# Kernel tuning notes

Measured on AMD Instinct MI355X. Metric: run time of the kernel, lower is better.

## Reference

```python
import jax, jax.numpy as jnp
import numpy as np

B, N, C, H = 16, 577, 384, 6
ONE_DIM = 24
RPD = 2 * ONE_DIM - 1  # 47
NUM_CLS = 1
HEAD_DIM = C // H
SCALE = HEAD_DIM ** -0.5


def _build_rel_pos_index():
    # Faithful to the torch loop: tmp[dy - y + off, dx - x + off] with
    # torch's negative-index wraparound -> modulo RPD.
    off = ONE_DIM // 2
    qy = np.repeat(np.arange(ONE_DIM), ONE_DIM)  # (Np,) y of each query patch
    qx = np.tile(np.arange(ONE_DIM), ONE_DIM)    # (Np,) x of each query patch
    ky, kx = qy, qx                              # key patches use same grid
    ry = (ky[None, :] - qy[:, None] + off) % RPD
    rx = (kx[None, :] - qx[:, None] + off) % RPD
    return jnp.asarray(ry * RPD + rx, dtype=jnp.int32)  # (Np, Np)


def setup_inputs() -> dict:
    key = jax.random.key(0)
    k = jax.random.split(key, 6)
    x = jax.random.normal(k[0], (B, N, C), dtype=jnp.float32)
    qkv_w = jax.random.normal(k[1], (3 * C, C), dtype=jnp.float32) * 0.02
    qkv_b = jnp.zeros((3 * C,), dtype=jnp.float32)
    proj_w = jax.random.normal(k[2], (C, C), dtype=jnp.float32) * 0.02
    proj_b = jnp.zeros((C,), dtype=jnp.float32)
    rel_pos = jax.random.normal(k[3], (H, RPD * RPD), dtype=jnp.float32) * 0.02
    mask = jax.random.randint(k[4], (B, N, N), 0, 2, dtype=jnp.int32)
    return {
        "x": x, "qkv_w": qkv_w, "qkv_b": qkv_b,
        "proj_w": proj_w, "proj_b": proj_b, "rel_pos": rel_pos,
        "rel_pos_index": _build_rel_pos_index(),
        "mask": mask, "patch_attn": 1,
    }


def reference(x, qkv_w, qkv_b, proj_w, proj_b, rel_pos, rel_pos_index, mask, patch_attn):
    # qkv projection: torch Linear -> x @ W^T + b
    qkv = x @ qkv_w.T + qkv_b                               # (B, N, 3C)
    qkv = qkv.reshape(B, N, 3, H, HEAD_DIM).transpose(2, 0, 3, 1, 4)
    q, k, v = qkv[0], qkv[1], qkv[2]                        # (B, H, N, hd)

    attn = jnp.einsum("bhqd,bhkd->bhqk", q, k) * SCALE      # (B, H, N, N)

    if patch_attn:
        # gather per-head relative-position bias for patch tokens
        bias = rel_pos[:, rel_pos_index]                    # (H, Np, Np)
        attn = attn.at[:, :, NUM_CLS:, NUM_CLS:].add(bias)

    neg = jnp.finfo(attn.dtype).min
    attn = jnp.where(mask[:, None, :, :] == 0, neg, attn)   # broadcast over heads

    attn = jax.nn.softmax(attn, axis=-1)
    out = jnp.einsum("bhqk,bhkd->bhqd", attn, v)            # (B, H, N, hd)
    out = out.transpose(0, 2, 1, 3).reshape(B, N, C)
    out = out @ proj_w.T + proj_b
    return out
```

## Files before the change

kernel.cpp:

```cpp
#include <hip/hip_runtime.h>
#include <float.h>
#include <math.h>

#define NB 16
#define NN 577
#define NC 384
#define NH 6
#define ND 64
#define RPD2 2209
#define MTOT 9232
#define MPAD 9344
#define SCALE_ 0.125f
#define NEGBIG -3.0e38f
#define BSTRIDE 580
#define NKPAD 640

typedef __attribute__((ext_vector_type(8))) short bf16x8;
typedef __attribute__((ext_vector_type(4))) float f32x4;
typedef unsigned short u16;

#define MFMA16(a, b, c) __builtin_amdgcn_mfma_f32_16x16x32_bf16(a, b, c, 0, 0, 0)

#define SQA 3932160ull
#define OFF_QH 0ull
#define OFF_QL SQA
#define OFF_KH (2ull * SQA)
#define OFF_KL (3ull * SQA)
#define OFF_VTH (4ull * SQA)
#define OFF_VTL (5ull * SQA)
#define OFF_XH (6ull * SQA)
#define OFF_XL (6ull * SQA + 3588096ull)
#define OFF_WQH (6ull * SQA + 2ull * 3588096ull)
#define OFF_WQL (OFF_WQH + 442368ull)
#define OFF_WPH (OFF_WQL + 442368ull)
#define OFF_WPL (OFF_WPH + 147456ull)
#define OFF_BT  (OFF_WPL + 147456ull)
#define OFF_PM  (OFF_BT + 2007960ull)

static __device__ __forceinline__ u16 f2bf(float f) {
  unsigned u = __float_as_uint(f);
  u += 0x7fff + ((u >> 16) & 1);
  return (u16)(u >> 16);
}
static __device__ __forceinline__ float bf2f(u16 h) {
  return __uint_as_float((unsigned)h << 16);
}
static __device__ __forceinline__ void split2(float v, u16& hi, u16& lo) {
  hi = f2bf(v);
  lo = f2bf(v - bf2f(hi));
}
static __device__ __forceinline__ void gload16(const void* g, void* l) {
  __builtin_amdgcn_global_load_lds(
      (const __attribute__((address_space(1))) void*)g,
      (__attribute__((address_space(3))) void*)l, 16, 0, 0);
}

__global__ __launch_bounds__(256) void split_inputs_k(
    const float* __restrict__ x, const float* __restrict__ wq,
    const float* __restrict__ wp, u16* __restrict__ ws)
{
  const int q = blockIdx.x * 256 + threadIdx.x;
  float4 v = {0.f, 0.f, 0.f, 0.f};
  u16 *dh, *dl;
  if (q < 897024) {
    if (q < 886272) v = ((const float4*)x)[q];
    dh = ws + OFF_XH + 4ull * q;
    dl = ws + OFF_XL + 4ull * q;
  } else if (q < 1007616) {
    int t = q - 897024;
    v = ((const float4*)wq)[t];
    dh = ws + OFF_WQH + 4ull * t;
    dl = ws + OFF_WQL + 4ull * t;
  } else {
    int t = q - 1007616;
    v = ((const float4*)wp)[t];
    dh = ws + OFF_WPH + 4ull * t;
    dl = ws + OFF_WPL + 4ull * t;
  }
  ushort4 hh, ll;
  split2(v.x, hh.x, ll.x);
  split2(v.y, hh.y, ll.y);
  split2(v.z, hh.z, ll.z);
  split2(v.w, hh.w, ll.w);
  *(ushort4*)dh = hh;
  *(ushort4*)dl = ll;
}

__global__ __launch_bounds__(256) void pack_mask_k(const int* __restrict__ mask,
                                                   unsigned* __restrict__ pm)
{
  const int wid = (blockIdx.x * 256 + threadIdx.x) >> 6;
  const int lane = threadIdx.x & 63;
  if (wid >= MTOT) return;
  const int* mr = mask + (size_t)wid * NN;
#pragma unroll
  for (int c = 0; c < 10; ++c) {
    int k = c * 64 + lane;
    int v = (k < NN) ? mr[k] : 0;
    unsigned long long bal = __ballot(v != 0);
    if (lane == 0) pm[wid * 20 + 2 * c] = (unsigned)bal;
    if (lane == 1) pm[wid * 20 + 2 * c + 1] = (unsigned)(bal >> 32);
  }
}

__global__ __launch_bounds__(256) void bias_build_k(
    const float* __restrict__ rel_pos, const int* __restrict__ rel_idx,
    const int* __restrict__ patch, u16* __restrict__ tbl)
{
  const int q = blockIdx.x;
  const int h = blockIdx.y;
  const int pa = *patch;
  u16* row = tbl + ((size_t)h * NN + q) * BSTRIDE;
  for (int kk = threadIdx.x; kk < BSTRIDE; kk += 256) {
    float v = 0.f;
    if (pa && q >= 1 && kk >= 1 && kk < NN)
      v = rel_pos[h * RPD2 + rel_idx[(q - 1) * 576 + (kk - 1)]];
    row[kk] = f2bf(v);
  }
}

__global__ __launch_bounds__(256, 3) void qkv_mfma_k(
    const u16* __restrict__ Xh, const u16* __restrict__ Xl,
    const u16* __restrict__ Wh, const u16* __restrict__ Wl,
    const float* __restrict__ bias, u16* __restrict__ ws)
{
  __shared__ u16 Ash[2][4096], Asl[2][4096];

  const int tid = threadIdx.x;
  const int w = tid >> 6, l = tid & 63, lq = l & 15, lg = l >> 4;
  const int wm = (w >> 1) * 64, wn = (w & 1) * 64;
  const int mb = blockIdx.x * 128;
  const int rb = blockIdx.y * 128;
  const int r0 = rb + wn;
  const int soff = (l >> 2) * 384 + (l & 3) * 8;

#define STAGE_A(k0_, bf_)                                                    \
  {                                                                          \
    _Pragma("unroll")                                                        \
    for (int j = 0; j < 2; ++j) {                                            \
      const int tr = 32 * w + 16 * j;                                        \
      const size_t ga = (size_t)(mb + tr) * 384 + (k0_) + soff;              \
      gload16(&Xh[ga], &Ash[bf_][tr * 32]);                                  \
      gload16(&Xl[ga], &Asl[bf_][tr * 32]);                                  \
    }                                                                        \
  }

  STAGE_A(0, 0);

  f32x4 acc[4][4];
#pragma unroll
  for (int nt = 0; nt < 4; ++nt) {
    float bv = bias[r0 + 16 * nt + lq];
#pragma unroll
    for (int mt = 0; mt < 4; ++mt) acc[mt][nt] = (f32x4){bv, bv, bv, bv};
  }

  const size_t brow = (size_t)(r0 + lq) * 384 + 8 * lg;
  for (int k0 = 0; k0 < 384; k0 += 32) {
    const int bf = (k0 >> 5) & 1;
    __syncthreads();
    if (k0 < 352) STAGE_A(k0 + 32, bf ^ 1);

    bf16x8 bhf[4], blf[4];
#pragma unroll
    for (int nt = 0; nt < 4; ++nt) {
      bhf[nt] = *(const bf16x8*)&Wh[brow + (size_t)(16 * nt) * 384 + k0];
      blf[nt] = *(const bf16x8*)&Wl[brow + (size_t)(16 * nt) * 384 + k0];
    }
#pragma unroll
    for (int mt = 0; mt < 4; ++mt) {
      bf16x8 ah = *(const bf16x8*)&Ash[bf][(wm + 16 * mt + lq) * 32 + 8 * lg];
      bf16x8 al = *(const bf16x8*)&Asl[bf][(wm + 16 * mt + lq) * 32 + 8 * lg];
#pragma unroll
      for (int nt = 0; nt < 4; ++nt) {
        acc[mt][nt] = MFMA16(ah, bhf[nt], acc[mt][nt]);
        acc[mt][nt] = MFMA16(ah, blf[nt], acc[mt][nt]);
        acc[mt][nt] = MFMA16(al, bhf[nt], acc[mt][nt]);
      }
    }
  }
#undef STAGE_A

  const int comp = rb / 384;
  const int h = ((rb % 384) + wn) >> 6;
#pragma unroll
  for (int mt = 0; mt < 4; ++mt)
#pragma unroll
    for (int r = 0; r < 4; ++r) {
      int m = mb + wm + 16 * mt + 4 * lg + r;
      if (m >= MTOT) continue;
      int bb = m / NN, nn = m - bb * NN;
      int bh = bb * NH + h;
#pragma unroll
      for (int nt = 0; nt < 4; ++nt) {
        int d = 16 * nt + lq;
        float v = acc[mt][nt][r];
        u16 hi, lo;
        if (comp == 0) {
          v *= SCALE_;
          split2(v, hi, lo);
          size_t a = ((size_t)bh * NKPAD + nn) * 64 + d;
          ws[OFF_QH + a] = hi;
          ws[OFF_QL + a] = lo;
        } else if (comp == 1) {
          split2(v, hi, lo);
          size_t a = ((size_t)bh * NKPAD + nn) * 64 + d;
          ws[OFF_KH + a] = hi;
          ws[OFF_KL + a] = lo;
        } else {
          split2(v, hi, lo);
          size_t a = ((size_t)bh * 64 + d) * NKPAD + nn;
          ws[OFF_VTH + a] = hi;
          ws[OFF_VTL + a] = lo;
        }
      }
    }
}

__global__ __launch_bounds__(256, 2) void attn_k(
    const u16* __restrict__ Qh, const u16* __restrict__ Ql,
    const u16* __restrict__ Kh, const u16* __restrict__ Kl,
    const u16* __restrict__ Vth, const u16* __restrict__ Vtl,
    const u16* __restrict__ btbl, const unsigned* __restrict__ pm,
    u16* __restrict__ Oh, u16* __restrict__ Ol)
{
  __shared__ u16 Kth[2][4096], Ktl[2][4096];
  __shared__ u16 Vsh[2][4096], Vsl[2][4096];
  __shared__ u16 Ph[4][2048];

  const int tid = threadIdx.x;
  const int w = tid >> 6, l = tid & 63, lq = l & 15, lg = l >> 4;
  const int q0 = blockIdx.x * 128;
  const int h = blockIdx.y, b = blockIdx.z;
  const int bh = b * NH + h;
  const int qr0 = q0 + 32 * w + lq;
  const int qr1 = qr0 + 16;
  const int swz = (lq & 7) << 3;
  const int ln8 = l >> 3, lc8 = l & 7;
  const int koff = ln8 * 64 + ((lc8 ^ ln8) << 3);
  const int voff = ln8 * NKPAD + ((lc8 ^ ln8) << 3);

#define STAGE(ch, bf)                                                        \
  {                                                                          \
    const int kb_ = (ch) * 64;                                               \
    const size_t kgb = ((size_t)bh * NKPAD + kb_ + 16 * w) * 64 + koff;      \
    const size_t vgb = ((size_t)bh * 64 + 16 * w) * NKPAD + kb_ + voff;      \
    gload16(&Kh[kgb],              &Kth[bf][(16 * w) * 64]);                 \
    gload16(&Kh[kgb + 512],        &Kth[bf][(16 * w + 8) * 64]);             \
    gload16(&Kl[kgb],              &Ktl[bf][(16 * w) * 64]);                 \
    gload16(&Kl[kgb + 512],        &Ktl[bf][(16 * w + 8) * 64]);             \
    gload16(&Vth[vgb],             &Vsh[bf][(16 * w) * 64]);                 \
    gload16(&Vth[vgb + 8 * NKPAD], &Vsh[bf][(16 * w + 8) * 64]);             \
    gload16(&Vtl[vgb],             &Vsl[bf][(16 * w) * 64]);                 \
    gload16(&Vtl[vgb + 8 * NKPAD], &Vsl[bf][(16 * w + 8) * 64]);             \
  }

  STAGE(0, 0);

  const size_t qb0 = ((size_t)bh * NKPAD + qr0) * 64 + 8 * lg;
  const size_t qb1 = ((size_t)bh * NKPAD + qr1) * 64 + 8 * lg;
  bf16x8 q0h[2], q0l[2], q1h[2], q1l[2];
  q0h[0] = *(const bf16x8*)&Qh[qb0];
  q0h[1] = *(const bf16x8*)&Qh[qb0 + 32];
  q0l[0] = *(const bf16x8*)&Ql[qb0];
  q0l[1] = *(const bf16x8*)&Ql[qb0 + 32];
  q1h[0] = *(const bf16x8*)&Qh[qb1];
  q1h[1] = *(const bf16x8*)&Qh[qb1 + 32];
  q1l[0] = *(const bf16x8*)&Ql[qb1];
  q1l[1] = *(const bf16x8*)&Ql[qb1 + 32];

  const int gq0 = (qr0 < NN) ? qr0 : NN - 1;
  const int gq1 = (qr1 < NN) ? qr1 : NN - 1;
  const bool qv0 = qr0 < NN, qv1 = qr1 < NN;
  const unsigned* pmrow0 = pm + ((size_t)b * NN + gq0) * 20;
  const unsigned* pmrow1 = pm + ((size_t)b * NN + gq1) * 20;
  const size_t brow0 = ((size_t)h * NN + gq0) * BSTRIDE;
  const size_t brow1 = ((size_t)h * NN + gq1) * BSTRIDE;

  float m_reg0 = NEGBIG, l_reg0 = 0.f;
  float m_reg1 = NEGBIG, l_reg1 = 0.f;
  f32x4 accO0[4] = {}, accO1[4] = {};

  for (int ch = 0; ch < 10; ++ch) {
    const int kb = ch * 64;
    const int bf = ch & 1;
    __syncthreads();
    if (ch < 9) STAGE(ch + 1, bf ^ 1);

    unsigned long long m64_0 = (unsigned long long)pmrow0[2 * ch] |
                               ((unsigned long long)pmrow0[2 * ch + 1] << 32);
    unsigned long long m64_1 = (unsigned long long)pmrow1[2 * ch] |
                               ((unsigned long long)pmrow1[2 * ch + 1] << 32);
    f32x4 ci0[4], ci1[4];
#pragma unroll
    for (int t = 0; t < 4; ++t) {
      ci0[t] = (f32x4){0.f, 0.f, 0.f, 0.f};
      ci1[t] = (f32x4){0.f, 0.f, 0.f, 0.f};
      int kkb = kb + 16 * t + 4 * lg;
      if (kkb <= 576) {
        if (qv0) {
          ushort4 b4 = *(const ushort4*)&btbl[brow0 + kkb];
          ci0[t][0] = bf2f(b4.x); ci0[t][1] = bf2f(b4.y);
          ci0[t][2] = bf2f(b4.z); ci0[t][3] = bf2f(b4.w);
        }
        if (qv1) {
          ushort4 b4 = *(const ushort4*)&btbl[brow1 + kkb];
          ci1[t][0] = bf2f(b4.x); ci1[t][1] = bf2f(b4.y);
          ci1[t][2] = bf2f(b4.z); ci1[t][3] = bf2f(b4.w);
        }
      }
    }

    float sv0[4][4], sv1[4][4];
#pragma unroll
    for (int t = 0; t < 4; ++t) {
      f32x4 a0 = ci0[t], a1 = ci1[t];
      const int ar = (16 * t + lq) * 64;
#pragma unroll
      for (int ks = 0; ks < 2; ++ks) {
        const int c = (8 * lg + 32 * ks) ^ swz;
        bf16x8 ah = *(const bf16x8*)&Kth[bf][ar + c];
        bf16x8 al = *(const bf16x8*)&Ktl[bf][ar + c];
        a0 = MFMA16(ah, q0h[ks], a0);
        a0 = MFMA16(ah, q0l[ks], a0);
        a0 = MFMA16(al, q0h[ks], a0);
        a1 = MFMA16(ah, q1h[ks], a1);
        a1 = MFMA16(ah, q1l[ks], a1);
        a1 = MFMA16(al, q1h[ks], a1);
      }
#pragma unroll
      for (int r = 0; r < 4; ++r) { sv0[t][r] = a0[r]; sv1[t][r] = a1[r]; }
    }

    {
      float cmax = NEGBIG;
#pragma unroll
      for (int t = 0; t < 4; ++t)
#pragma unroll
        for (int r = 0; r < 4; ++r) {
          int kl = 16 * t + 4 * lg + r;
          float s = ((m64_0 >> kl) & 1ull) ? sv0[t][r] : NEGBIG;
          sv0[t][r] = s;
          cmax = fmaxf(cmax, s);
        }
      cmax = fmaxf(cmax, __shfl_xor(cmax, 16));
      cmax = fmaxf(cmax, __shfl_xor(cmax, 32));
      float m_new = fmaxf(m_reg0, cmax);
      float fx = __expf(m_reg0 - m_new);
      float csum = 0.f;
#pragma unroll
      for (int t = 0; t < 4; ++t) {
        float e0 = __expf(sv0[t][0] - m_new);
        float e1 = __expf(sv0[t][1] - m_new);
        float e2 = __expf(sv0[t][2] - m_new);
        float e3 = __expf(sv0[t][3] - m_new);
        csum += e0 + e1 + e2 + e3;
        ushort4 ph;
        ph.x = f2bf(e0); ph.y = f2bf(e1); ph.z = f2bf(e2); ph.w = f2bf(e3);
        *(ushort4*)&Ph[w][lq * 64 + ((16 * t + 4 * lg) ^ swz)] = ph;
      }
      csum += __shfl_xor(csum, 16);
      csum += __shfl_xor(csum, 32);
      l_reg0 = l_reg0 * fx + csum;
      m_reg0 = m_new;
      float fxr[4];
#pragma unroll
      for (int r = 0; r < 4; ++r) fxr[r] = __shfl(fx, 4 * lg + r);
#pragma unroll
      for (int t = 0; t < 4; ++t) {
        accO0[t][0] *= fxr[0]; accO0[t][1] *= fxr[1];
        accO0[t][2] *= fxr[2]; accO0[t][3] *= fxr[3];
      }
    }
    {
      float cmax = NEGBIG;
#pragma unroll
      for (int t = 0; t < 4; ++t)
#pragma unroll
        for (int r = 0; r < 4; ++r) {
          int kl = 16 * t + 4 * lg + r;
          float s = ((m64_1 >> kl) & 1ull) ? sv1[t][r] : NEGBIG;
          sv1[t][r] = s;
          cmax = fmaxf(cmax, s);
        }
      cmax = fmaxf(cmax, __shfl_xor(cmax, 16));
      cmax = fmaxf(cmax, __shfl_xor(cmax, 32));
      float m_new = fmaxf(m_reg1, cmax);
      float fx = __expf(m_reg1 - m_new);
      float csum = 0.f;
#pragma unroll
      for (int t = 0; t < 4; ++t) {
        float e0 = __expf(sv1[t][0] - m_new);
        float e1 = __expf(sv1[t][1] - m_new);
        float e2 = __expf(sv1[t][2] - m_new);
        float e3 = __expf(sv1[t][3] - m_new);
        csum += e0 + e1 + e2 + e3;
        ushort4 ph;
        ph.x = f2bf(e0); ph.y = f2bf(e1); ph.z = f2bf(e2); ph.w = f2bf(e3);
        *(ushort4*)&Ph[w][(16 + lq) * 64 + ((16 * t + 4 * lg) ^ swz)] = ph;
      }
      csum += __shfl_xor(csum, 16);
      csum += __shfl_xor(csum, 32);
      l_reg1 = l_reg1 * fx + csum;
      m_reg1 = m_new;
      float fxr[4];
#pragma unroll
      for (int r = 0; r < 4; ++r) fxr[r] = __shfl(fx, 4 * lg + r);
#pragma unroll
      for (int t = 0; t < 4; ++t) {
        accO1[t][0] *= fxr[0]; accO1[t][1] *= fxr[1];
        accO1[t][2] *= fxr[2]; accO1[t][3] *= fxr[3];
      }
    }

    bf16x8 pa0[2], pa1[2];
#pragma unroll
    for (int ks = 0; ks < 2; ++ks) {
      int c = (8 * lg + 32 * ks) ^ swz;
      pa0[ks] = *(const bf16x8*)&Ph[w][lq * 64 + c];
      pa1[ks] = *(const bf16x8*)&Ph[w][(16 + lq) * 64 + c];
    }

#pragma unroll
    for (int t = 0; t < 4; ++t) {
      const int vr = (16 * t + lq) * 64;
#pragma unroll
      for (int ks = 0; ks < 2; ++ks) {
        const int c = (8 * lg + 32 * ks) ^ swz;
        bf16x8 vh = *(const bf16x8*)&Vsh[bf][vr + c];
        bf16x8 vl = *(const bf16x8*)&Vsl[bf][vr + c];
        accO0[t] = MFMA16(pa0[ks], vh, accO0[t]);
        accO0[t] = MFMA16(pa0[ks], vl, accO0[t]);
        accO1[t] = MFMA16(pa1[ks], vh, accO1[t]);
        accO1[t] = MFMA16(pa1[ks], vl, accO1[t]);
      }
    }
  }
#undef STAGE

  float il0 = 1.f / l_reg0;
  float il1 = 1.f / l_reg1;
  float ilr0[4], ilr1[4];
#pragma unroll
  for (int r = 0; r < 4; ++r) {
    ilr0[r] = __shfl(il0, 4 * lg + r);
    ilr1[r] = __shfl(il1, 4 * lg + r);
  }
#pragma unroll
  for (int t = 0; t < 4; ++t)
#pragma unroll
    for (int r = 0; r < 4; ++r) {
      int g0 = q0 + 32 * w + 4 * lg + r;
      if (g0 < NN) {
        float v = accO0[t][r] * ilr0[r];
        u16 hi, lo;
        split2(v, hi, lo);
        size_t a = ((size_t)b * NN + g0) * NC + h * 64 + 16 * t + lq;
        Oh[a] = hi;
        Ol[a] = lo;
      }
      int g1 = g0 + 16;
      if (g1 < NN) {
        float v = accO1[t][r] * ilr1[r];
        u16 hi, lo;
        split2(v, hi, lo);
        size_t a = ((size_t)b * NN + g1) * NC + h * 64 + 16 * t + lq;
        Oh[a] = hi;
        Ol[a] = lo;
      }
    }
}

__global__ __launch_bounds__(256, 3) void proj_mfma_k(
    const u16* __restrict__ Ah, const u16* __restrict__ Al,
    const u16* __restrict__ Wh, const u16* __restrict__ Wl,
    const float* __restrict__ bias, float* __restrict__ out)
{
  __shared__ u16 Ash[2][4096], Asl[2][4096];

  const int tid = threadIdx.x;
  const int w = tid >> 6, l = tid & 63, lq = l & 15, lg = l >> 4;
  const int wm = (w >> 1) * 64, wn = (w & 1) * 64;
  const int mb = blockIdx.x * 128;
  const int rb = blockIdx.y * 128;
  const int r0 = rb + wn;
  const int soff = (l >> 2) * 384 + (l & 3) * 8;

#define STAGE_A(k0_, bf_)                                                    \
  {                                                                          \
    _Pragma("unroll")                                                        \
    for (int j = 0; j < 2; ++j) {                                            \
      const int tr = 32 * w + 16 * j;                                        \
      const size_t ga = (size_t)(mb + tr) * 384 + (k0_) + soff;              \
      gload16(&Ah[ga], &Ash[bf_][tr * 32]);                                  \
      gload16(&Al[ga], &Asl[bf_][tr * 32]);                                  \
    }                                                                        \
  }

  STAGE_A(0, 0);

  f32x4 acc[4][4];
#pragma unroll
  for (int nt = 0; nt < 4; ++nt) {
    float bv = bias[r0 + 16 * nt + lq];
#pragma unroll
    for (int mt = 0; mt < 4; ++mt) acc[mt][nt] = (f32x4){bv, bv, bv, bv};
  }

  const size_t brow = (size_t)(r0 + lq) * 384 + 8 * lg;
  for (int k0 = 0; k0 < 384; k0 += 32) {
    const int bf = (k0 >> 5) & 1;
    __syncthreads();
    if (k0 < 352) STAGE_A(k0 + 32, bf ^ 1);

    bf16x8 bhf[4], blf[4];
#pragma unroll
    for (int nt = 0; nt < 4; ++nt) {
      bhf[nt] = *(const bf16x8*)&Wh[brow + (size_t)(16 * nt) * 384 + k0];
      blf[nt] = *(const bf16x8*)&Wl[brow + (size_t)(16 * nt) * 384 + k0];
    }
#pragma unroll
    for (int mt = 0; mt < 4; ++mt) {
      bf16x8 ah = *(const bf16x8*)&Ash[bf][(wm + 16 * mt + lq) * 32 + 8 * lg];
      bf16x8 al = *(const bf16x8*)&Asl[bf][(wm + 16 * mt + lq) * 32 + 8 * lg];
#pragma unroll
      for (int nt = 0; nt < 4; ++nt) {
        acc[mt][nt] = MFMA16(ah, bhf[nt], acc[mt][nt]);
        acc[mt][nt] = MFMA16(ah, blf[nt], acc[mt][nt]);
        acc[mt][nt] = MFMA16(al, bhf[nt], acc[mt][nt]);
      }
    }
  }
#undef STAGE_A

#pragma unroll
  for (int mt = 0; mt < 4; ++mt)
#pragma unroll
    for (int r = 0; r < 4; ++r) {
      int m = mb + wm + 16 * mt + 4 * lg + r;
      if (m >= MTOT) continue;
#pragma unroll
      for (int nt = 0; nt < 4; ++nt)
        out[(size_t)m * NC + r0 + 16 * nt + lq] = acc[mt][nt][r];
    }
}

extern "C" void kernel_launch(void* const* d_in, const int* in_sizes, int n_in,
                              void* d_out, int out_size, void* d_ws, size_t ws_size,
                              hipStream_t stream) {
  const float* x       = (const float*)d_in[0];
  const float* qkv_w   = (const float*)d_in[1];
  const float* qkv_b   = (const float*)d_in[2];
  const float* proj_w  = (const float*)d_in[3];
  const float* proj_b  = (const float*)d_in[4];
  const float* rel_pos = (const float*)d_in[5];
  const int*   rel_idx = (const int*)d_in[6];
  const int*   mask    = (const int*)d_in[7];
  const int*   patch   = (const int*)d_in[8];
  float* out = (float*)d_out;
  u16* W16 = (u16*)d_ws;

  unsigned* pmp = (unsigned*)(W16 + OFF_PM);
  u16* btblp = W16 + OFF_BT;

  split_inputs_k<<<4080, 256, 0, stream>>>(x, qkv_w, proj_w, W16);
  pack_mask_k<<<2308, 256, 0, stream>>>(mask, pmp);
  bias_build_k<<<dim3(NN, NH), 256, 0, stream>>>(rel_pos, rel_idx, patch, btblp);
  qkv_mfma_k<<<dim3(73, 9), 256, 0, stream>>>(
      W16 + OFF_XH, W16 + OFF_XL, W16 + OFF_WQH, W16 + OFF_WQL, qkv_b, W16);
  attn_k<<<dim3(5, NH, NB), 256, 0, stream>>>(
      W16 + OFF_QH, W16 + OFF_QL, W16 + OFF_KH, W16 + OFF_KL,
      W16 + OFF_VTH, W16 + OFF_VTL, btblp, pmp,
      W16 + OFF_XH, W16 + OFF_XL);
  proj_mfma_k<<<dim3(73, 3), 256, 0, stream>>>(
      W16 + OFF_XH, W16 + OFF_XL, W16 + OFF_WPH, W16 + OFF_WPL, proj_b, out);
}
```

Measured before the change: 179.4 us.

## Stage GEMM weights in LDS and prefetch attention mask/bias one chunk ahead

The QKV and projection GEMMs now stage the weight tiles (hi/lo bf16 halves) into double-buffered LDS through the async copy path, so they are no longer read straight from global memory inside the k loop. Their occupancy hint drops from 3 to 2 blocks per CU to fit the larger LDS footprint. The attention kernel now loads the next chunk's mask bits and relative-position bias one iteration ahead in registers, and raises wave priority around the MFMA sections. This is meant to hide global load latency, at the cost of more LDS, more registers and lower occupancy.

```diff
diff --git a/kernel.cpp b/kernel.cpp
--- a/kernel.cpp
+++ b/kernel.cpp
@@ -119,12 +119,13 @@
   }
 }
 
-__global__ __launch_bounds__(256, 3) void qkv_mfma_k(
+__global__ __launch_bounds__(256, 2) void qkv_mfma_k(
     const u16* __restrict__ Xh, const u16* __restrict__ Xl,
     const u16* __restrict__ Wh, const u16* __restrict__ Wl,
     const float* __restrict__ bias, u16* __restrict__ ws)
 {
   __shared__ u16 Ash[2][4096], Asl[2][4096];
+  __shared__ u16 Bsh[2][4096], Bsl[2][4096];
 
   const int tid = threadIdx.x;
   const int w = tid >> 6, l = tid & 63, lq = l & 15, lg = l >> 4;
@@ -134,18 +135,21 @@
   const int r0 = rb + wn;
   const int soff = (l >> 2) * 384 + (l & 3) * 8;
 
-#define STAGE_A(k0_, bf_)                                                    \
+#define STAGE_AB(k0_, bf_)                                                   \
   {                                                                          \
     _Pragma("unroll")                                                        \
     for (int j = 0; j < 2; ++j) {                                            \
       const int tr = 32 * w + 16 * j;                                        \
       const size_t ga = (size_t)(mb + tr) * 384 + (k0_) + soff;              \
+      const size_t gb = (size_t)(rb + tr) * 384 + (k0_) + soff;              \
       gload16(&Xh[ga], &Ash[bf_][tr * 32]);                                  \
       gload16(&Xl[ga], &Asl[bf_][tr * 32]);                                  \
+      gload16(&Wh[gb], &Bsh[bf_][tr * 32]);                                  \
+      gload16(&Wl[gb], &Bsl[bf_][tr * 32]);                                  \
     }                                                                        \
   }
 
-  STAGE_A(0, 0);
+  STAGE_AB(0, 0);
 
   f32x4 acc[4][4];
 #pragma unroll
@@ -155,22 +159,21 @@
     for (int mt = 0; mt < 4; ++mt) acc[mt][nt] = (f32x4){bv, bv, bv, bv};
   }
 
-  const size_t brow = (size_t)(r0 + lq) * 384 + 8 * lg;
   for (int k0 = 0; k0 < 384; k0 += 32) {
-    const int bf = (k0 >> 5) & 1;
+    const int bfb = (k0 >> 5) & 1;
     __syncthreads();
-    if (k0 < 352) STAGE_A(k0 + 32, bf ^ 1);
+    if (k0 < 352) STAGE_AB(k0 + 32, bfb ^ 1);
 
     bf16x8 bhf[4], blf[4];
 #pragma unroll
     for (int nt = 0; nt < 4; ++nt) {
-      bhf[nt] = *(const bf16x8*)&Wh[brow + (size_t)(16 * nt) * 384 + k0];
-      blf[nt] = *(const bf16x8*)&Wl[brow + (size_t)(16 * nt) * 384 + k0];
+      bhf[nt] = *(const bf16x8*)&Bsh[bfb][(wn + 16 * nt + lq) * 32 + 8 * lg];
+      blf[nt] = *(const bf16x8*)&Bsl[bfb][(wn + 16 * nt + lq) * 32 + 8 * lg];
     }
 #pragma unroll
     for (int mt = 0; mt < 4; ++mt) {
-      bf16x8 ah = *(const bf16x8*)&Ash[bf][(wm + 16 * mt + lq) * 32 + 8 * lg];
-      bf16x8 al = *(const bf16x8*)&Asl[bf][(wm + 16 * mt + lq) * 32 + 8 * lg];
+      bf16x8 ah = *(const bf16x8*)&Ash[bfb][(wm + 16 * mt + lq) * 32 + 8 * lg];
+      bf16x8 al = *(const bf16x8*)&Asl[bfb][(wm + 16 * mt + lq) * 32 + 8 * lg];
 #pragma unroll
       for (int nt = 0; nt < 4; ++nt) {
         acc[mt][nt] = MFMA16(ah, bhf[nt], acc[mt][nt]);
@@ -179,7 +182,7 @@
       }
     }
   }
-#undef STAGE_A
+#undef STAGE_AB
 
   const int comp = rb / 384;
   const int h = ((rb % 384) + wn) >> 6;
@@ -277,44 +280,59 @@
   const size_t brow0 = ((size_t)h * NN + gq0) * BSTRIDE;
   const size_t brow1 = ((size_t)h * NN + gq1) * BSTRIDE;
 
+  uint2 cM0, cM1, nM0, nM1;
+  uint2 cB0[4], cB1[4], nB0[4], nB1[4];
+  cM0 = *(const uint2*)&pmrow0[0];
+  cM1 = *(const uint2*)&pmrow1[0];
+#pragma unroll
+  for (int t = 0; t < 4; ++t) {
+    int kkb = 16 * t + 4 * lg;
+    cB0[t] = (qv0 && kkb <= 576) ? *(const uint2*)&btbl[brow0 + kkb]
+                                 : make_uint2(0u, 0u);
+    cB1[t] = (qv1 && kkb <= 576) ? *(const uint2*)&btbl[brow1 + kkb]
+                                 : make_uint2(0u, 0u);
+  }
+
   float m_reg0 = NEGBIG, l_reg0 = 0.f;
   float m_reg1 = NEGBIG, l_reg1 = 0.f;
   f32x4 accO0[4] = {}, accO1[4] = {};
 
   for (int ch = 0; ch < 10; ++ch) {
-    const int kb = ch * 64;
     const int bf = ch & 1;
     __syncthreads();
-    if (ch < 9) STAGE(ch + 1, bf ^ 1);
-
-    unsigned long long m64_0 = (unsigned long long)pmrow0[2 * ch] |
-                               ((unsigned long long)pmrow0[2 * ch + 1] << 32);
-    unsigned long long m64_1 = (unsigned long long)pmrow1[2 * ch] |
-                               ((unsigned long long)pmrow1[2 * ch + 1] << 32);
-    f32x4 ci0[4], ci1[4];
+    if (ch < 9) {
+      nM0 = *(const uint2*)&pmrow0[2 * (ch + 1)];
+      nM1 = *(const uint2*)&pmrow1[2 * (ch + 1)];
+      const int kb2 = (ch + 1) * 64;
+#pragma unroll
+      for (int t = 0; t < 4; ++t) {
+        int kkb = kb2 + 16 * t + 4 * lg;
+        nB0[t] = (qv0 && kkb <= 576) ? *(const uint2*)&btbl[brow0 + kkb]
+                                     : make_uint2(0u, 0u);
+        nB1[t] = (qv1 && kkb <= 576) ? *(const uint2*)&btbl[brow1 + kkb]
+                                     : make_uint2(0u, 0u);
+      }
+      STAGE(ch + 1, bf ^ 1);
+    }
+
+    unsigned long long m64_0 = (unsigned long long)cM0.x |
+                               ((unsigned long long)cM0.y << 32);
+    unsigned long long m64_1 = (unsigned long long)cM1.x |
+                               ((unsigned long long)cM1.y << 32);
+
+    float sv0[4][4], sv1[4][4];
+    __builtin_amdgcn_s_setprio(1);
 #pragma unroll
     for (int t = 0; t < 4; ++t) {
-      ci0[t] = (f32x4){0.f, 0.f, 0.f, 0.f};
-      ci1[t] = (f32x4){0.f, 0.f, 0.f, 0.f};
-      int kkb = kb + 16 * t + 4 * lg;
-      if (kkb <= 576) {
-        if (qv0) {
-          ushort4 b4 = *(const ushort4*)&btbl[brow0 + kkb];
-          ci0[t][0] = bf2f(b4.x); ci0[t][1] = bf2f(b4.y);
-          ci0[t][2] = bf2f(b4.z); ci0[t][3] = bf2f(b4.w);
-        }
-        if (qv1) {
-          ushort4 b4 = *(const ushort4*)&btbl[brow1 + kkb];
-          ci1[t][0] = bf2f(b4.x); ci1[t][1] = bf2f(b4.y);
-          ci1[t][2] = bf2f(b4.z); ci1[t][3] = bf2f(b4.w);
-        }
-      }
-    }
-
-    float sv0[4][4], sv1[4][4];
-#pragma unroll
-    for (int t = 0; t < 4; ++t) {
-      f32x4 a0 = ci0[t], a1 = ci1[t];
+      f32x4 a0, a1;
+      a0[0] = bf2f((u16)(cB0[t].x & 0xffff));
+      a0[1] = bf2f((u16)(cB0[t].x >> 16));
+      a0[2] = bf2f((u16)(cB0[t].y & 0xffff));
+      a0[3] = bf2f((u16)(cB0[t].y >> 16));
+      a1[0] = bf2f((u16)(cB1[t].x & 0xffff));
+      a1[1] = bf2f((u16)(cB1[t].x >> 16));
+      a1[2] = bf2f((u16)(cB1[t].y & 0xffff));
+      a1[3] = bf2f((u16)(cB1[t].y >> 16));
       const int ar = (16 * t + lq) * 64;
 #pragma unroll
       for (int ks = 0; ks < 2; ++ks) {
@@ -331,6 +349,7 @@
 #pragma unroll
       for (int r = 0; r < 4; ++r) { sv0[t][r] = a0[r]; sv1[t][r] = a1[r]; }
     }
+    __builtin_amdgcn_s_setprio(0);
 
     {
       float cmax = NEGBIG;
@@ -421,6 +440,7 @@
       pa1[ks] = *(const bf16x8*)&Ph[w][(16 + lq) * 64 + c];
     }
 
+    __builtin_amdgcn_s_setprio(1);
 #pragma unroll
     for (int t = 0; t < 4; ++t) {
       const int vr = (16 * t + lq) * 64;
@@ -434,6 +454,13 @@
         accO1[t] = MFMA16(pa1[ks], vh, accO1[t]);
         accO1[t] = MFMA16(pa1[ks], vl, accO1[t]);
       }
+    }
+    __builtin_amdgcn_s_setprio(0);
+
+    if (ch < 9) {
+      cM0 = nM0; cM1 = nM1;
+#pragma unroll
+      for (int t = 0; t < 4; ++t) { cB0[t] = nB0[t]; cB1[t] = nB1[t]; }
     }
   }
 #undef STAGE
@@ -471,12 +498,13 @@
     }
 }
 
-__global__ __launch_bounds__(256, 3) void proj_mfma_k(
+__global__ __launch_bounds__(256, 2) void proj_mfma_k(
     const u16* __restrict__ Ah, const u16* __restrict__ Al,
     const u16* __restrict__ Wh, const u16* __restrict__ Wl,
     const float* __restrict__ bias, float* __restrict__ out)
 {
   __shared__ u16 Ash[2][4096], Asl[2][4096];
+  __shared__ u16 Bsh[2][4096], Bsl[2][4096];
 
   const int tid = threadIdx.x;
   const int w = tid >> 6, l = tid & 63, lq = l & 15, lg = l >> 4;
@@ -486,18 +514,21 @@
   const int r0 = rb + wn;
   const int soff = (l >> 2) * 384 + (l & 3) * 8;
 
-#define STAGE_A(k0_, bf_)                                                    \
+#define STAGE_AB(k0_, bf_)                                                   \
   {                                                                          \
     _Pragma("unroll")                                                        \
     for (int j = 0; j < 2; ++j) {                                            \
       const int tr = 32 * w + 16 * j;                                        \
       const size_t ga = (size_t)(mb + tr) * 384 + (k0_) + soff;              \
+      const size_t gb = (size_t)(rb + tr) * 384 + (k0_) + soff;              \
       gload16(&Ah[ga], &Ash[bf_][tr * 32]);                                  \
       gload16(&Al[ga], &Asl[bf_][tr * 32]);                                  \
+      gload16(&Wh[gb], &Bsh[bf_][tr * 32]);                                  \
+      gload16(&Wl[gb], &Bsl[bf_][tr * 32]);                                  \
     }                                                                        \
   }
 
-  STAGE_A(0, 0);
+  STAGE_AB(0, 0);
 
   f32x4 acc[4][4];
 #pragma unroll
@@ -507,22 +538,21 @@
     for (int mt = 0; mt < 4; ++mt) acc[mt][nt] = (f32x4){bv, bv, bv, bv};
   }
 
-  const size_t brow = (size_t)(r0 + lq) * 384 + 8 * lg;
   for (int k0 = 0; k0 < 384; k0 += 32) {
-    const int bf = (k0 >> 5) & 1;
+    const int bfb = (k0 >> 5) & 1;
     __syncthreads();
-    if (k0 < 352) STAGE_A(k0 + 32, bf ^ 1);
+    if (k0 < 352) STAGE_AB(k0 + 32, bfb ^ 1);
 
     bf16x8 bhf[4], blf[4];
 #pragma unroll
     for (int nt = 0; nt < 4; ++nt) {
-      bhf[nt] = *(const bf16x8*)&Wh[brow + (size_t)(16 * nt) * 384 + k0];
-      blf[nt] = *(const bf16x8*)&Wl[brow + (size_t)(16 * nt) * 384 + k0];
+      bhf[nt] = *(const bf16x8*)&Bsh[bfb][(wn + 16 * nt + lq) * 32 + 8 * lg];
+      blf[nt] = *(const bf16x8*)&Bsl[bfb][(wn + 16 * nt + lq) * 32 + 8 * lg];
     }
 #pragma unroll
     for (int mt = 0; mt < 4; ++mt) {
-      bf16x8 ah = *(const bf16x8*)&Ash[bf][(wm + 16 * mt + lq) * 32 + 8 * lg];
-      bf16x8 al = *(const bf16x8*)&Asl[bf][(wm + 16 * mt + lq) * 32 + 8 * lg];
+      bf16x8 ah = *(const bf16x8*)&Ash[bfb][(wm + 16 * mt + lq) * 32 + 8 * lg];
+      bf16x8 al = *(const bf16x8*)&Asl[bfb][(wm + 16 * mt + lq) * 32 + 8 * lg];
 #pragma unroll
       for (int nt = 0; nt < 4; ++nt) {
         acc[mt][nt] = MFMA16(ah, bhf[nt], acc[mt][nt]);
@@ -531,7 +561,7 @@
       }
     }
   }
-#undef STAGE_A
+#undef STAGE_AB
 
 #pragma unroll
   for (int mt = 0; mt < 4; ++mt)
```

New measurement: 164.3 us. 1.09x faster.
